# Optimization experiments

Hardware: AMD Instinct MI355X
Metric: run time of the kernel (lower is better)

## Reference

```python
import jax, jax.numpy as jnp
import numpy as np
from jax.scipy.special import logsumexp

TEMPERATURE = 0.07
ALPHA = 0.5
THRESHOLD1 = 0.5
THRESHOLD2 = 0.3


def setup_inputs() -> dict:
    key = jax.random.key(0)
    k1, k2, k3 = jax.random.split(key, 3)
    B, D = 8192, 256
    f_img = jax.random.normal(k1, (B, D), dtype=jnp.float32)
    f_txt = jax.random.normal(k2, (B, D), dtype=jnp.float32)
    scores = jax.random.uniform(k3, (B, B), dtype=jnp.float32)
    return {"f_img": f_img, "f_txt": f_txt, "scores": scores}


def _l2norm(x):
    # torch F.normalize(p=2, dim=1)
    return x / jnp.linalg.norm(x, axis=1, keepdims=True)


def _per_row_loss(logits, pos, neg, n_neg):
    # For each row l and each positive column j, the torch code builds the
    # vector [logits[l,j], logits[l,neg]] and takes -log_softmax(...)[0]
    # divided by its length (1 + n_neg[l]). Vectorized:
    neg_lse = logsumexp(jnp.where(neg, logits, -jnp.inf), axis=-1, keepdims=True)  # [B,1]
    lse = jnp.logaddexp(logits, neg_lse)                                           # [B,B]
    per_pos = (lse - logits) / (1.0 + n_neg)[:, None]                              # -logprob/len
    row = jnp.sum(per_pos * pos, axis=-1) / jnp.sum(pos, axis=-1)                  # mean over pos
    return jnp.sum(row) / logits.shape[0]


def reference(f_img, f_txt, scores):
    fi = _l2norm(f_img)
    ft = _l2norm(f_txt)
    logits_i2t = jnp.matmul(fi, ft.T) / TEMPERATURE  # [B,B]
    logits_t2i = jnp.matmul(ft, fi.T) / TEMPERATURE  # [B,B]
    pos = (scores > THRESHOLD1).astype(logits_i2t.dtype)
    neg = scores <= THRESHOLD2
    n_neg = jnp.sum(neg, axis=-1).astype(logits_i2t.dtype)  # [B]
    loss_i2t = _per_row_loss(logits_i2t, pos, neg, n_neg)
    loss_t2i = _per_row_loss(logits_t2i, pos, neg, n_neg)
    return ALPHA * loss_i2t + (1.0 - ALPHA) * loss_t2i
```

## Files before the change

kernel.cpp:

```cpp
#include <hip/hip_runtime.h>
#include <stdint.h>
#include <stddef.h>

typedef _Float16 f16;
typedef _Float16 f16x8 __attribute__((ext_vector_type(8)));
typedef _Float16 f16x4 __attribute__((ext_vector_type(4)));
typedef float f32x4 __attribute__((ext_vector_type(4)));

#define NB 8192
#define DK 256

template<int CTRL>
__device__ __forceinline__ float dpp_add(float x) {
  int yi = __builtin_amdgcn_mov_dpp(__float_as_int(x), CTRL, 0xF, 0xF, true);
  return x + __int_as_float(yi);
}
__device__ __forceinline__ float reduce16(float x) {
  x = dpp_add<0xB1>(x);
  x = dpp_add<0x4E>(x);
  x = dpp_add<0x141>(x);
  x = dpp_add<0x140>(x);
  return x;
}

__global__ __launch_bounds__(256) void prep_kernel(const float* __restrict__ f_img,
                                                   const float* __restrict__ f_txt,
                                                   f16* __restrict__ fi16,
                                                   f16* __restrict__ ft16) {
  const int wave = threadIdx.x >> 6, lane = threadIdx.x & 63;
  const int row = blockIdx.x * 4 + wave;
  const float* src = (row < NB) ? f_img : f_txt;
  f16* dst = (row < NB) ? fi16 : ft16;
  const int r = row & (NB - 1);
  const float4 v = *reinterpret_cast<const float4*>(src + (size_t)r * DK + lane * 4);
  float ss = v.x * v.x + v.y * v.y + v.z * v.z + v.w * v.w;
  #pragma unroll
  for (int d = 1; d < 64; d <<= 1) ss += __shfl_xor(ss, d, 64);
  const float sc = 3.7796447300922722f / sqrtf(ss);
  f16x4 o;
  o[0] = (f16)(v.x * sc); o[1] = (f16)(v.y * sc);
  o[2] = (f16)(v.z * sc); o[3] = (f16)(v.w * sc);
  *reinterpret_cast<f16x4*>(dst + (size_t)r * DK + lane * 4) = o;
}

template<int PASS>
__global__ __launch_bounds__(256, 2) void hloss_tile(
    const f16* __restrict__ fi16, const f16* __restrict__ ft16,
    const float* __restrict__ scores,
    float* __restrict__ s_row, float* __restrict__ s_col,
    float* __restrict__ cnt_neg, float* __restrict__ cnt_pos,
    const float* __restrict__ nl_row, const float* __restrict__ nl_col,
    float* __restrict__ acc_i2t, float* __restrict__ acc_t2i)
{
  __shared__ __align__(16) char smem[65536];
  const int bid = blockIdx.x;
  const int swz = (bid & 7) * 512 + (bid >> 3);
  const int rt = swz >> 6, ct = swz & 63;
  const int row0 = rt << 7, col0 = ct << 7;
  const int tid = threadIdx.x;
  const int wave = tid >> 6, lane = tid & 63;
  const int wr = wave >> 1, wc = wave & 1;

  f32x4 acc1[4][4], acc2[4][4];
  #pragma unroll
  for (int m = 0; m < 4; ++m)
    #pragma unroll
    for (int n = 0; n < 4; ++n) {
      acc1[m][n] = {0.f, 0.f, 0.f, 0.f};
      acc2[m][n] = {0.f, 0.f, 0.f, 0.f};
    }

  const f16* psrc = (wave == 0) ? (fi16 + (size_t)row0 * DK)
                  : (wave == 1) ? (ft16 + (size_t)col0 * DK)
                  : (wave == 2) ? (ft16 + (size_t)row0 * DK)
                                : (fi16 + (size_t)col0 * DK);
  char* const pbase = smem + (wave << 14);
  const int sub = lane >> 3;
  const int sslot = ((lane & 7) ^ sub) << 4;

  const int fr = lane & 15;
  const int fg = lane >> 4;
  const int rswz = (fr & 7) << 4;

  for (int kt = 0; kt < 4; ++kt) {
    __syncthreads();
    #pragma unroll
    for (int i = 0; i < 16; ++i) {
      const char* g = (const char*)psrc + (((i << 3) + sub) << 9) + (kt << 7) + sslot;
      __builtin_amdgcn_global_load_lds(
          (const __attribute__((address_space(1))) uint32_t*)g,
          (__attribute__((address_space(3))) uint32_t*)(pbase + (i << 10)),
          16, 0, 0);
    }
    __syncthreads();
    #pragma unroll
    for (int ks = 0; ks < 2; ++ks) {
      const int koff = ((ks << 6) + (fg << 4)) ^ rswz;
      {
        f16x8 a[4], b[4];
        #pragma unroll
        for (int m = 0; m < 4; ++m) {
          a[m] = *reinterpret_cast<const f16x8*>(smem + (((wr << 6) + (m << 4) + fr) << 7) + koff);
          b[m] = *reinterpret_cast<const f16x8*>(smem + 16384 + (((wc << 6) + (m << 4) + fr) << 7) + koff);
        }
        #pragma unroll
        for (int m = 0; m < 4; ++m)
          #pragma unroll
          for (int n = 0; n < 4; ++n)
            acc1[m][n] = __builtin_amdgcn_mfma_f32_16x16x32_f16(a[m], b[n], acc1[m][n], 0, 0, 0);
      }
      {
        f16x8 a[4], b[4];
        #pragma unroll
        for (int m = 0; m < 4; ++m) {
          a[m] = *reinterpret_cast<const f16x8*>(smem + 32768 + (((wr << 6) + (m << 4) + fr) << 7) + koff);
          b[m] = *reinterpret_cast<const f16x8*>(smem + 49152 + (((wc << 6) + (m << 4) + fr) << 7) + koff);
        }
        #pragma unroll
        for (int m = 0; m < 4; ++m)
          #pragma unroll
          for (int n = 0; n < 4; ++n)
            acc2[m][n] = __builtin_amdgcn_mfma_f32_16x16x32_f16(a[m], b[n], acc2[m][n], 0, 0, 0);
      }
    }
  }

  const int rbase = row0 + (wr << 6) + (fg << 2);
  const int cbase = col0 + (wc << 6) + fr;

  #pragma unroll
  for (int m = 0; m < 4; ++m) {
    #pragma unroll
    for (int reg = 0; reg < 4; ++reg) {
      const int rg = rbase + (m << 4) + reg;
      if (PASS == 1) {
        float v1 = 0.f, v2 = 0.f, cnp = 0.f;
        #pragma unroll
        for (int n = 0; n < 4; ++n) {
          const float scv = __builtin_nontemporal_load(&scores[(size_t)rg * NB + cbase + (n << 4)]);
          const bool nb = (scv <= 0.3f);
          v1 += nb ? __expf(acc1[m][n][reg]) : 0.f;
          v2 += nb ? __expf(acc2[m][n][reg]) : 0.f;
          cnp += (nb ? 1.f : 0.f) + ((scv > 0.5f) ? 256.f : 0.f);
        }
        v1 = reduce16(v1); v2 = reduce16(v2); cnp = reduce16(cnp);
        if (fr == 0) {
          atomicAdd(&s_row[rg], v1);
          atomicAdd(&s_col[rg], v2);
          const float cp = floorf(cnp * (1.f / 256.f));
          atomicAdd(&cnt_neg[rg], cnp - 256.f * cp);
          atomicAdd(&cnt_pos[rg], cp);
        }
      } else {
        const float nlr = nl_row[rg];
        const float nlc = nl_col[rg];
        float v1 = 0.f, v2 = 0.f;
        #pragma unroll
        for (int n = 0; n < 4; ++n) {
          const float scv = __builtin_nontemporal_load(&scores[(size_t)rg * NB + cbase + (n << 4)]);
          const bool pb = (scv > 0.5f);
          const float z1 = nlr - acc1[m][n][reg];
          const float z2 = nlc - acc2[m][n][reg];
          const float t1 = fmaxf(z1, 0.f) + __logf(1.f + __expf(-fabsf(z1)));
          const float t2 = fmaxf(z2, 0.f) + __logf(1.f + __expf(-fabsf(z2)));
          v1 += pb ? t1 : 0.f;
          v2 += pb ? t2 : 0.f;
        }
        v1 = reduce16(v1); v2 = reduce16(v2);
        if (fr == 0) {
          atomicAdd(&acc_i2t[rg], v1);
          atomicAdd(&acc_t2i[rg], v2);
        }
      }
    }
  }
}

__global__ __launch_bounds__(256) void mid_kernel(const float* __restrict__ s_row,
                                                  const float* __restrict__ s_col,
                                                  float* __restrict__ nl_row,
                                                  float* __restrict__ nl_col) {
  const int i = blockIdx.x * 256 + threadIdx.x;
  nl_row[i] = logf(s_row[i]);
  nl_col[i] = logf(s_col[i]);
}

__global__ __launch_bounds__(256) void final_kernel(const float* __restrict__ acc_i2t,
                                                    const float* __restrict__ acc_t2i,
                                                    const float* __restrict__ cnt_neg,
                                                    const float* __restrict__ cnt_pos,
                                                    float* __restrict__ out) {
  float t = 0.f;
  for (int i = threadIdx.x; i < NB; i += 256) {
    const float denom = (1.0f + cnt_neg[i]) * cnt_pos[i];
    t += 0.5f * (acc_i2t[i] + acc_t2i[i]) / denom;
  }
  #pragma unroll
  for (int d = 1; d < 64; d <<= 1) t += __shfl_xor(t, d, 64);
  __shared__ float wsum[4];
  if ((threadIdx.x & 63) == 0) wsum[threadIdx.x >> 6] = t;
  __syncthreads();
  if (threadIdx.x == 0)
    out[0] = (wsum[0] + wsum[1] + wsum[2] + wsum[3]) * (1.0f / (float)NB);
}

extern "C" void kernel_launch(void* const* d_in, const int* in_sizes, int n_in,
                              void* d_out, int out_size, void* d_ws, size_t ws_size,
                              hipStream_t stream) {
  (void)in_sizes; (void)n_in; (void)out_size; (void)ws_size;
  const float* f_img  = (const float*)d_in[0];
  const float* f_txt  = (const float*)d_in[1];
  const float* scores = (const float*)d_in[2];

  char* ws = (char*)d_ws;
  f16* fi16 = (f16*)ws;
  f16* ft16 = (f16*)(ws + (size_t)(4 << 20));
  float* s_row   = (float*)(ws + (size_t)(8 << 20));
  float* s_col   = s_row + NB;
  float* cnt_neg = s_row + 2 * NB;
  float* cnt_pos = s_row + 3 * NB;
  float* acc_i2t = s_row + 4 * NB;
  float* acc_t2i = s_row + 5 * NB;
  float* nl_row  = s_row + 6 * NB;
  float* nl_col  = s_row + 7 * NB;

  (void)hipMemsetAsync(s_row, 0, 6 * NB * sizeof(float), stream);
  hipLaunchKernelGGL(prep_kernel, dim3(4096), dim3(256), 0, stream, f_img, f_txt, fi16, ft16);
  hipLaunchKernelGGL(HIP_KERNEL_NAME(hloss_tile<1>), dim3(4096), dim3(256), 0, stream,
                     fi16, ft16, scores, s_row, s_col, cnt_neg, cnt_pos,
                     nl_row, nl_col, acc_i2t, acc_t2i);
  hipLaunchKernelGGL(mid_kernel, dim3(32), dim3(256), 0, stream, s_row, s_col, nl_row, nl_col);
  hipLaunchKernelGGL(HIP_KERNEL_NAME(hloss_tile<2>), dim3(4096), dim3(256), 0, stream,
                     fi16, ft16, scores, s_row, s_col, cnt_neg, cnt_pos,
                     nl_row, nl_col, acc_i2t, acc_t2i);
  hipLaunchKernelGGL(final_kernel, dim3(1), dim3(256), 0, stream,
                     acc_i2t, acc_t2i, cnt_neg, cnt_pos, (float*)d_out);
}
```

Baseline: 820.7 us.

## Pack positive mask as bits in pass one; prefetch scores during GEMM

Pass 1 now issues the scores loads inside the k-loop, so they overlap with the LDS fills and MFMAs. It also writes a 1-bit-per-element positive mask built with ballot. Pass 2 reads this 8 MB bitmask instead of re-reading the 256 MB scores matrix, which cuts its HBM traffic by roughly a factor of 32. The final reduction is spread over 32 blocks that combine with atomicAdd into a zeroed output. The cost is more live registers for the prefetched scores in pass 1 and an extra memset.

After: 1.016 ms. +23.7%, slower.

```diff
diff --git a/kernel.cpp b/kernel.cpp
--- a/kernel.cpp
+++ b/kernel.cpp
@@ -43,12 +43,128 @@
   *reinterpret_cast<f16x4*>(dst + (size_t)r * DK + lane * 4) = o;
 }
 
-template<int PASS>
-__global__ __launch_bounds__(256, 2) void hloss_tile(
+
+__global__ __launch_bounds__(256, 2) void hloss_pass1(
     const f16* __restrict__ fi16, const f16* __restrict__ ft16,
     const float* __restrict__ scores,
     float* __restrict__ s_row, float* __restrict__ s_col,
     float* __restrict__ cnt_neg, float* __restrict__ cnt_pos,
+    uint8_t* __restrict__ posmask)
+{
+  __shared__ __align__(16) char smem[65536];
+  const int bid = blockIdx.x;
+  const int swz = (bid & 7) * 512 + (bid >> 3);
+  const int rt = swz >> 6, ct = swz & 63;
+  const int row0 = rt << 7, col0 = ct << 7;
+  const int tid = threadIdx.x;
+  const int wave = tid >> 6, lane = tid & 63;
+  const int wr = wave >> 1, wc = wave & 1;
+
+  f32x4 acc1[4][4], acc2[4][4];
+  #pragma unroll
+  for (int m = 0; m < 4; ++m)
+    #pragma unroll
+    for (int n = 0; n < 4; ++n) { acc1[m][n] = {0,0,0,0}; acc2[m][n] = {0,0,0,0}; }
+
+  const f16* psrc = (wave == 0) ? (fi16 + (size_t)row0 * DK)
+                  : (wave == 1) ? (ft16 + (size_t)col0 * DK)
+                  : (wave == 2) ? (ft16 + (size_t)row0 * DK)
+                                : (fi16 + (size_t)col0 * DK);
+  char* const pbase = smem + (wave << 14);
+  const int sub = lane >> 3;
+  const int sslot = ((lane & 7) ^ sub) << 4;
+
+  const int fr = lane & 15;
+  const int fg = lane >> 4;
+  const int rswz = (fr & 7) << 4;
+
+  const int rbase = row0 + (wr << 6) + (fg << 2);
+  const int cbase = col0 + (wc << 6) + fr;
+
+  float sc[4][4][4];
+
+  for (int kt = 0; kt < 4; ++kt) {
+    __syncthreads();
+    #pragma unroll
+    for (int i = 0; i < 16; ++i) {
+      const char* g = (const char*)psrc + (((i << 3) + sub) << 9) + (kt << 7) + sslot;
+      __builtin_amdgcn_global_load_lds(
+          (const __attribute__((address_space(1))) uint32_t*)g,
+          (__attribute__((address_space(3))) uint32_t*)(pbase + (i << 10)),
+          16, 0, 0);
+    }
+    #pragma unroll
+    for (int n = 0; n < 4; ++n)
+      #pragma unroll
+      for (int reg = 0; reg < 4; ++reg)
+        sc[kt][n][reg] = __builtin_nontemporal_load(
+            &scores[(size_t)(rbase + (kt << 4) + reg) * NB + cbase + (n << 4)]);
+    __syncthreads();
+    #pragma unroll
+    for (int ks = 0; ks < 2; ++ks) {
+      const int koff = ((ks << 6) + (fg << 4)) ^ rswz;
+      {
+        f16x8 a[4], b[4];
+        #pragma unroll
+        for (int m = 0; m < 4; ++m) {
+          a[m] = *reinterpret_cast<const f16x8*>(smem + (((wr << 6) + (m << 4) + fr) << 7) + koff);
+          b[m] = *reinterpret_cast<const f16x8*>(smem + 16384 + (((wc << 6) + (m << 4) + fr) << 7) + koff);
+        }
+        #pragma unroll
+        for (int m = 0; m < 4; ++m)
+          #pragma unroll
+          for (int n = 0; n < 4; ++n)
+            acc1[m][n] = __builtin_amdgcn_mfma_f32_16x16x32_f16(a[m], b[n], acc1[m][n], 0, 0, 0);
+      }
+      {
+        f16x8 a[4], b[4];
+        #pragma unroll
+        for (int m = 0; m < 4; ++m) {
+          a[m] = *reinterpret_cast<const f16x8*>(smem + 32768 + (((wr << 6) + (m << 4) + fr) << 7) + koff);
+          b[m] = *reinterpret_cast<const f16x8*>(smem + 49152 + (((wc << 6) + (m << 4) + fr) << 7) + koff);
+        }
+        #pragma unroll
+        for (int m = 0; m < 4; ++m)
+          #pragma unroll
+          for (int n = 0; n < 4; ++n)
+            acc2[m][n] = __builtin_amdgcn_mfma_f32_16x16x32_f16(a[m], b[n], acc2[m][n], 0, 0, 0);
+      }
+    }
+  }
+
+  #pragma unroll
+  for (int m = 0; m < 4; ++m) {
+    #pragma unroll
+    for (int reg = 0; reg < 4; ++reg) {
+      const int rg = rbase + (m << 4) + reg;
+      float v1 = 0.f, v2 = 0.f, cnp = 0.f;
+      uint64_t w = 0;
+      #pragma unroll
+      for (int n = 0; n < 4; ++n) {
+        const float scv = sc[m][n][reg];
+        const bool nb = (scv <= 0.3f);
+        v1 += nb ? __expf(acc1[m][n][reg]) : 0.f;
+        v2 += nb ? __expf(acc2[m][n][reg]) : 0.f;
+        cnp += (nb ? 1.f : 0.f) + ((scv > 0.5f) ? 256.f : 0.f);
+        const uint64_t bal = __ballot(scv > 0.5f);
+        w |= ((bal >> (fg << 4)) & 0xFFFFull) << (n << 4);
+      }
+      v1 = reduce16(v1); v2 = reduce16(v2); cnp = reduce16(cnp);
+      if (fr == 0) {
+        atomicAdd(&s_row[rg], v1);
+        atomicAdd(&s_col[rg], v2);
+        const float cp = floorf(cnp * (1.f / 256.f));
+        atomicAdd(&cnt_neg[rg], cnp - 256.f * cp);
+        atomicAdd(&cnt_pos[rg], cp);
+        *reinterpret_cast<uint64_t*>(posmask + (size_t)rg * (NB / 8) + (col0 >> 3) + (wc << 3)) = w;
+      }
+    }
+  }
+}
+
+__global__ __launch_bounds__(256, 2) void hloss_pass2(
+    const f16* __restrict__ fi16, const f16* __restrict__ ft16,
+    const uint8_t* __restrict__ posmask,
     const float* __restrict__ nl_row, const float* __restrict__ nl_col,
     float* __restrict__ acc_i2t, float* __restrict__ acc_t2i)
 {
@@ -65,10 +181,7 @@
   #pragma unroll
   for (int m = 0; m < 4; ++m)
     #pragma unroll
-    for (int n = 0; n < 4; ++n) {
-      acc1[m][n] = {0.f, 0.f, 0.f, 0.f};
-      acc2[m][n] = {0.f, 0.f, 0.f, 0.f};
-    }
+    for (int n = 0; n < 4; ++n) { acc1[m][n] = {0,0,0,0}; acc2[m][n] = {0,0,0,0}; }
 
   const f16* psrc = (wave == 0) ? (fi16 + (size_t)row0 * DK)
                   : (wave == 1) ? (ft16 + (size_t)col0 * DK)
@@ -82,6 +195,21 @@
   const int fg = lane >> 4;
   const int rswz = (fr & 7) << 4;
 
+  const int rbase = row0 + (wr << 6) + (fg << 2);
+
+  uint64_t mk[4][4];
+  float nlr[4][4], nlc[4][4];
+  #pragma unroll
+  for (int m = 0; m < 4; ++m)
+    #pragma unroll
+    for (int reg = 0; reg < 4; ++reg) {
+      const int rg = rbase + (m << 4) + reg;
+      mk[m][reg] = *reinterpret_cast<const uint64_t*>(
+          posmask + (size_t)rg * (NB / 8) + (col0 >> 3) + (wc << 3));
+      nlr[m][reg] = nl_row[rg];
+      nlc[m][reg] = nl_col[rg];
+    }
+
   for (int kt = 0; kt < 4; ++kt) {
     __syncthreads();
     #pragma unroll
@@ -125,52 +253,28 @@
     }
   }
 
-  const int rbase = row0 + (wr << 6) + (fg << 2);
-  const int cbase = col0 + (wc << 6) + fr;
-
   #pragma unroll
   for (int m = 0; m < 4; ++m) {
     #pragma unroll
     for (int reg = 0; reg < 4; ++reg) {
       const int rg = rbase + (m << 4) + reg;
-      if (PASS == 1) {
-        float v1 = 0.f, v2 = 0.f, cnp = 0.f;
-        #pragma unroll
-        for (int n = 0; n < 4; ++n) {
-          const float scv = __builtin_nontemporal_load(&scores[(size_t)rg * NB + cbase + (n << 4)]);
-          const bool nb = (scv <= 0.3f);
-          v1 += nb ? __expf(acc1[m][n][reg]) : 0.f;
-          v2 += nb ? __expf(acc2[m][n][reg]) : 0.f;
-          cnp += (nb ? 1.f : 0.f) + ((scv > 0.5f) ? 256.f : 0.f);
-        }
-        v1 = reduce16(v1); v2 = reduce16(v2); cnp = reduce16(cnp);
-        if (fr == 0) {
-          atomicAdd(&s_row[rg], v1);
-          atomicAdd(&s_col[rg], v2);
-          const float cp = floorf(cnp * (1.f / 256.f));
-          atomicAdd(&cnt_neg[rg], cnp - 256.f * cp);
-          atomicAdd(&cnt_pos[rg], cp);
-        }
-      } else {
-        const float nlr = nl_row[rg];
-        const float nlc = nl_col[rg];
-        float v1 = 0.f, v2 = 0.f;
-        #pragma unroll
-        for (int n = 0; n < 4; ++n) {
-          const float scv = __builtin_nontemporal_load(&scores[(size_t)rg * NB + cbase + (n << 4)]);
-          const bool pb = (scv > 0.5f);
-          const float z1 = nlr - acc1[m][n][reg];
-          const float z2 = nlc - acc2[m][n][reg];
-          const float t1 = fmaxf(z1, 0.f) + __logf(1.f + __expf(-fabsf(z1)));
-          const float t2 = fmaxf(z2, 0.f) + __logf(1.f + __expf(-fabsf(z2)));
-          v1 += pb ? t1 : 0.f;
-          v2 += pb ? t2 : 0.f;
-        }
-        v1 = reduce16(v1); v2 = reduce16(v2);
-        if (fr == 0) {
-          atomicAdd(&acc_i2t[rg], v1);
-          atomicAdd(&acc_t2i[rg], v2);
-        }
+      const float vnlr = nlr[m][reg], vnlc = nlc[m][reg];
+      const uint64_t w = mk[m][reg];
+      float v1 = 0.f, v2 = 0.f;
+      #pragma unroll
+      for (int n = 0; n < 4; ++n) {
+        const bool pb = (w >> ((n << 4) + fr)) & 1ull;
+        const float z1 = vnlr - acc1[m][n][reg];
+        const float z2 = vnlc - acc2[m][n][reg];
+        const float t1 = fmaxf(z1, 0.f) + __logf(1.f + __expf(-fabsf(z1)));
+        const float t2 = fmaxf(z2, 0.f) + __logf(1.f + __expf(-fabsf(z2)));
+        v1 += pb ? t1 : 0.f;
+        v2 += pb ? t2 : 0.f;
+      }
+      v1 = reduce16(v1); v2 = reduce16(v2);
+      if (fr == 0) {
+        atomicAdd(&acc_i2t[rg], v1);
+        atomicAdd(&acc_t2i[rg], v2);
       }
     }
   }
@@ -190,18 +294,16 @@
                                                     const float* __restrict__ cnt_neg,
                                                     const float* __restrict__ cnt_pos,
                                                     float* __restrict__ out) {
-  float t = 0.f;
-  for (int i = threadIdx.x; i < NB; i += 256) {
-    const float denom = (1.0f + cnt_neg[i]) * cnt_pos[i];
-    t += 0.5f * (acc_i2t[i] + acc_t2i[i]) / denom;
-  }
+  const int i = blockIdx.x * 256 + threadIdx.x;
+  const float denom = (1.0f + cnt_neg[i]) * cnt_pos[i];
+  float t = 0.5f * (acc_i2t[i] + acc_t2i[i]) / denom;
   #pragma unroll
   for (int d = 1; d < 64; d <<= 1) t += __shfl_xor(t, d, 64);
   __shared__ float wsum[4];
   if ((threadIdx.x & 63) == 0) wsum[threadIdx.x >> 6] = t;
   __syncthreads();
   if (threadIdx.x == 0)
-    out[0] = (wsum[0] + wsum[1] + wsum[2] + wsum[3]) * (1.0f / (float)NB);
+    atomicAdd(out, (wsum[0] + wsum[1] + wsum[2] + wsum[3]) * (1.0f / (float)NB));
 }
 
 extern "C" void kernel_launch(void* const* d_in, const int* in_sizes, int n_in,
@@ -223,16 +325,16 @@
   float* acc_t2i = s_row + 5 * NB;
   float* nl_row  = s_row + 6 * NB;
   float* nl_col  = s_row + 7 * NB;
+  uint8_t* posmask = (uint8_t*)(ws + (size_t)(16 << 20));
 
   (void)hipMemsetAsync(s_row, 0, 6 * NB * sizeof(float), stream);
+  (void)hipMemsetAsync(d_out, 0, sizeof(float), stream);
   hipLaunchKernelGGL(prep_kernel, dim3(4096), dim3(256), 0, stream, f_img, f_txt, fi16, ft16);
-  hipLaunchKernelGGL(HIP_KERNEL_NAME(hloss_tile<1>), dim3(4096), dim3(256), 0, stream,
-                     fi16, ft16, scores, s_row, s_col, cnt_neg, cnt_pos,
-                     nl_row, nl_col, acc_i2t, acc_t2i);
+  hipLaunchKernelGGL(hloss_pass1, dim3(4096), dim3(256), 0, stream,
+                     fi16, ft16, scores, s_row, s_col, cnt_neg, cnt_pos, posmask);
   hipLaunchKernelGGL(mid_kernel, dim3(32), dim3(256), 0, stream, s_row, s_col, nl_row, nl_col);
-  hipLaunchKernelGGL(HIP_KERNEL_NAME(hloss_tile<2>), dim3(4096), dim3(256), 0, stream,
-                     fi16, ft16, scores, s_row, s_col, cnt_neg, cnt_pos,
-                     nl_row, nl_col, acc_i2t, acc_t2i);
-  hipLaunchKernelGGL(final_kernel, dim3(1), dim3(256), 0, stream,
+  hipLaunchKernelGGL(hloss_pass2, dim3(4096), dim3(256), 0, stream,
+                     fi16, ft16, posmask, nl_row, nl_col, acc_i2t, acc_t2i);
+  hipLaunchKernelGGL(final_kernel, dim3(32), dim3(256), 0, stream,
                      acc_i2t, acc_t2i, cnt_neg, cnt_pos, (float*)d_out);
 }
```
